# Kernel tuning notes

Hardware: AMD Instinct MI355X
Metric: run time of the kernel (lower is better)

The kernel has to match this reference:

```python
import jax, jax.numpy as jnp
import numpy as np
from jax import lax

PR = [0.0, -39.68, -3.0, 69.12, 39.68, 1.0]  # POINT_CLOUD_RANGE
SIZE = (1024, 1024)  # (W, H)
B = 4
NBF = 64
BN_EPS = 1e-5


def setup_inputs() -> dict:
    key = jax.random.key(0)
    ks = jax.random.split(key, 16)
    N = 800_000
    bidx = jax.random.randint(ks[0], (N,), 0, B).astype(jnp.float32)
    x = jax.random.uniform(ks[1], (N,), minval=PR[0], maxval=PR[3])
    y = jax.random.uniform(ks[2], (N,), minval=PR[1], maxval=PR[4])
    z = jax.random.uniform(ks[3], (N,), minval=PR[2], maxval=PR[5])
    inten = jax.random.uniform(ks[4], (N,))
    points = jnp.stack([bidx, x, y, z, inten], axis=1)
    params = {}
    chans = [(4, 8), (8, 16), (16, 32), (32, NBF)]
    for li, (ci, co) in enumerate(chans, start=1):
        kk = jax.random.split(ks[5 + li], 6)
        params[f"w{li}"] = jax.random.normal(kk[0], (co, ci, 3, 3)) * (1.0 / np.sqrt(ci * 9))
        params[f"b{li}"] = jax.random.normal(kk[1], (co,)) * 0.01
        params[f"g{li}"] = jax.random.uniform(kk[2], (co,), minval=0.5, maxval=1.5)
        params[f"be{li}"] = jax.random.normal(kk[3], (co,)) * 0.01
        params[f"m{li}"] = jax.random.normal(kk[4], (co,)) * 0.01
        params[f"v{li}"] = jax.random.uniform(kk[5], (co,), minval=0.5, maxval=1.5)
    return {"points": points, "batch_size": 4, **params}


def _points_to_bev(points, batch_size):
    # Faithful to points_to_bevs_all (returned channels: count/50, zmin, zmax, intensity;
    # bev_average_z is computed but never returned in the original, so it is omitted).
    W, H = SIZE
    xs = W / (PR[3] - PR[0])
    ys = H / (PR[4] - PR[1])
    # PR[0] == 0 branch of the original
    xp = (points[:, 1] * xs).astype(jnp.int32)
    yp = ((points[:, 2] + (PR[4] - PR[1]) / 2) * ys).astype(jnp.int32)
    b = points[:, 0].astype(jnp.int32)
    mask = (xp >= 0) & (xp < W) & (yp >= 0) & (yp < H)
    lin = jnp.where(mask, (b * H + yp) * W + xp, 0)  # flat [B*H*W] index
    z = points[:, 3]
    inten = points[:, 4]
    n = batch_size * H * W
    neg = jnp.float32(-jnp.inf)
    pos = jnp.float32(jnp.inf)
    cnt = jnp.zeros((n,), jnp.float32).at[lin].add(mask.astype(jnp.float32))
    zmax = jnp.full((n,), -10.0, jnp.float32).at[lin].max(jnp.where(mask, z, neg))
    zmin = jnp.full((n,), 10.0, jnp.float32).at[lin].min(jnp.where(mask, z, pos))
    iv = jnp.zeros((n,), jnp.float32).at[lin].max(jnp.where(mask, inten, neg))
    bev = jnp.where(cnt == 0, 1.0, cnt) / 50.0
    stacked = jnp.stack([bev, zmin, zmax, iv], axis=0).reshape(4, batch_size, H, W)
    return jnp.transpose(stacked, (1, 0, 2, 3))  # [B,4,H,W]


def _cbr(x, w, b, g, be, m, v):
    # Conv(3x3, stride 1, pad 1) + BatchNorm (inference) + ReLU
    y = lax.conv_general_dilated(x, w, (1, 1), 'SAME',
                                 dimension_numbers=('NCHW', 'OIHW', 'NCHW'))
    y = y + b[:, None, None]
    scale = (g / jnp.sqrt(v + BN_EPS))[:, None, None]
    y = (y - m[:, None, None]) * scale + be[:, None, None]
    return jax.nn.relu(y)


def _pool(x):
    return lax.reduce_window(x, -jnp.inf, lax.max, (1, 1, 2, 2), (1, 1, 2, 2), 'VALID')


def reference(points, batch_size,
              w1, b1, g1, be1, m1, v1,
              w2, b2, g2, be2, m2, v2,
              w3, b3, g3, be3, m3, v3,
              w4, b4, g4, be4, m4, v4):
    bev = _points_to_bev(points, batch_size)  # [B,4,1024,1024]
    x = _pool(_cbr(bev, w1, b1, g1, be1, m1, v1))  # [B,8,512,512]
    x = _pool(_cbr(x, w2, b2, g2, be2, m2, v2))    # [B,16,256,256]
    x = _pool(_cbr(x, w3, b3, g3, be3, m3, v3))    # [B,32,128,128]
    return _cbr(x, w4, b4, g4, be4, m4, v4)        # [B,64,128,128] spatial_features
```

## Files before the change

kernel.cpp:

```cpp
#include <hip/hip_runtime.h>
#include <cstdint>
#include <cstddef>

#define HH 1024
#define WW 1024
#define NB 4

typedef _Float16 half8 __attribute__((ext_vector_type(8)));
typedef float f32x4 __attribute__((ext_vector_type(4)));
typedef unsigned long long ull;

__global__ __launch_bounds__(256)
void clear_cells(float4* __restrict__ p, int n4) {
  int stride = gridDim.x * blockDim.x;
  float4 z; z.x = 0.f; z.y = 0.f; z.z = 0.f; z.w = 0.f;
  for (int i = blockIdx.x * blockDim.x + threadIdx.x; i < n4; i += stride)
    p[i] = z;
}

__device__ __forceinline__ unsigned merge_cell(unsigned a, unsigned zq,
                                               unsigned zn, unsigned iq) {
  unsigned cnt = a & 0xFFu;
  unsigned civ = (a >> 8) & 0xFFu;
  unsigned czn = (a >> 16) & 0xFFu;
  unsigned czx = a >> 24;
  cnt = (cnt < 255u) ? cnt + 1u : cnt;
  civ = civ > iq ? civ : iq;
  czn = czn > zn ? czn : zn;
  czx = czx > zq ? czx : zq;
  return cnt | (civ << 8) | (czn << 16) | (czx << 24);
}

__global__ __launch_bounds__(256)
void scatter_points_packed(const float* __restrict__ pts, int n,
                           unsigned* __restrict__ cell) {
  const float xs   = (float)(1024.0 / 69.12);
  const float ys   = (float)(1024.0 / (39.68 + 39.68));
  const float yoff = 39.68f;
  int i = blockIdx.x * blockDim.x + threadIdx.x;
  if (i >= n) return;
  float b  = pts[(size_t)i * 5 + 0];
  float x  = pts[(size_t)i * 5 + 1];
  float y  = pts[(size_t)i * 5 + 2];
  float z  = pts[(size_t)i * 5 + 3];
  float it = pts[(size_t)i * 5 + 4];
  int xp = (int)(x * xs);
  int yp = (int)((y + yoff) * ys);
  if (xp < 0 || xp >= WW || yp < 0 || yp >= HH) return;
  int lin = ((int)b * HH + yp) * WW + xp;

  float zc = fminf(fmaxf(z, -3.f), 1.f);
  unsigned zq = (unsigned)(int)((zc + 3.f) * (255.f / 4.f) + 0.5f);
  if (zq > 255u) zq = 255u;
  float ic = fminf(fmaxf(it, 0.f), 1.f);
  unsigned iq = (unsigned)(int)(ic * 255.f + 0.5f);
  if (iq > 255u) iq = 255u;
  unsigned zn = 255u - zq;

  unsigned g = atomicCAS(&cell[lin], 0u, merge_cell(0u, zq, zn, iq));
  while (g != 0u) {
    unsigned r = atomicCAS(&cell[lin], g, merge_cell(g, zq, zn, iq));
    if (r == g) break;
    g = r;
  }
}

template<int CI, int CIp, int COT, int COp, int HWI, int PXT, int KS,
         bool POOL, int INMODE, bool OUTCL>
__global__ __launch_bounds__(512)
void conv_mfma(const void* __restrict__ in, void* __restrict__ outv,
               const float* __restrict__ wgt, const float* __restrict__ bias,
               const float* __restrict__ gam, const float* __restrict__ bet,
               const float* __restrict__ mean, const float* __restrict__ var) {
  constexpr int PYT  = 32;
  constexpr int NTHR = 512;
  constexpr int NT   = COp / 16;
  constexpr int XH   = PXT / 16;
  constexpr int NCOL = PXT + 2;
  constexpr int NCELL = (PYT + 2) * NCOL;
  constexpr int WROW = KS * 32 + 8;
  constexpr int INE  = NCELL * CIp;
  constexpr int L2C  = (CIp == 8) ? 3 : ((CIp == 16) ? 4 : 5);
  constexpr int KTOT = 9 * CIp;
  constexpr int COR  = (COT < COp) ? COT : COp;
  constexpr int PXH  = PXT / 2;
  constexpr int OCS  = 136;
  static_assert(CIp % 8 == 0 && COp % 16 == 0, "");
  static_assert(!OUTCL || (POOL && COT % 8 == 0), "");
  static_assert(!POOL || 16 * PXH * COp * 2 <= INE * 2, "out overlay fits");
  static_assert(POOL || COp * OCS * 4 <= INE * 2, "out overlay fits");

  __shared__ __align__(16) char s_raw[INE * 2 + COp * WROW * 2 + COp * 8];
  _Float16* s_in = (_Float16*)s_raw;
  _Float16* s_w  = (_Float16*)(s_raw + INE * 2);
  float* s_scale = (float*)(s_raw + INE * 2 + (size_t)COp * WROW * 2);
  float* s_shift = s_scale + COp;

  const int cobase = blockIdx.y * COp;
  const int b = blockIdx.z;
  constexpr int NPX = HWI / PXT;
  const int pyi = blockIdx.x / NPX;
  const int pxi = blockIdx.x - pyi * NPX;
  const int y0 = pyi * PYT, x0 = pxi * PXT;

  half8 zv;
  #pragma unroll
  for (int q = 0; q < 8; ++q) zv[q] = (_Float16)0.f;

  if constexpr (INMODE == 0) {
    const unsigned* pin = (const unsigned*)in;
    for (int t = threadIdx.x; t < NCELL; t += NTHR) {
      int col = t % NCOL;
      int row = t / NCOL;
      int gy = y0 - 1 + row, gx = x0 - 1 + col;
      half8 v = zv;
      if (gy >= 0 && gy < HH && gx >= 0 && gx < WW) {
        unsigned pv = pin[((size_t)b * HH + gy) * WW + gx];
        unsigned cnt = pv & 0xFFu;
        unsigned ivq = (pv >> 8) & 0xFFu;
        unsigned znq = (pv >> 16) & 0xFFu;
        unsigned zxq = pv >> 24;
        float c0, c1, c2, c3;
        if (cnt == 0) { c0 = 0.02f; c1 = 10.f; c2 = -10.f; c3 = 0.f; }
        else {
          c0 = (float)cnt * 0.02f;
          c1 = (float)(255u - znq) * (4.0f / 255.0f) - 3.0f;
          c2 = (float)zxq * (4.0f / 255.0f) - 3.0f;
          c3 = (float)ivq * (1.0f / 255.0f);
        }
        v[0] = (_Float16)c0; v[1] = (_Float16)c1;
        v[2] = (_Float16)c2; v[3] = (_Float16)c3;
      }
      *(half8*)&s_in[(size_t)t * CIp] = v;
    }
  } else {
    const _Float16* fin = (const _Float16*)in;
    for (int t = threadIdx.x; t < NCELL; t += NTHR) {
      int col = t % NCOL;
      int row = t / NCOL;
      int gy = y0 - 1 + row, gx = x0 - 1 + col;
      bool okc = (gy >= 0 && gy < HWI && gx >= 0 && gx < HWI);
      int swz = (CIp == 8) ? 0 : ((CIp == 16) ? ((col >> 2) & 1) : ((col >> 1) & 3));
      #pragma unroll
      for (int c8 = 0; c8 < CIp / 8; ++c8) {
        half8 v = zv;
        if (okc)
          v = *(const half8*)((const _Float16*)fin +
                (((size_t)b * HWI + gy) * HWI + gx) * CI + c8 * 8);
        *(half8*)&s_in[(size_t)t * CIp + ((c8 ^ swz) << 3)] = v;
      }
    }
  }
  for (int t = threadIdx.x; t < COp * KS * 32; t += NTHR) {
    int k   = t % (KS * 32);
    int col = t / (KS * 32);
    int cog = cobase + col;
    float v = 0.f;
    if (k < KTOT && cog < COT) {
      int tap = k / CIp, ci = k % CIp;
      if (ci < CI) v = wgt[((size_t)cog * CI + ci) * 9 + tap];
    }
    s_w[col * WROW + k] = (_Float16)v;
  }
  if (threadIdx.x < COp) {
    int col = threadIdx.x;
    int cog = cobase + col;
    float sc = 0.f, sh = 0.f;
    if (cog < COT) {
      sc = gam[cog] / sqrtf(var[cog] + 1e-5f);
      sh = (bias[cog] - mean[cog]) * sc + bet[cog];
    }
    s_scale[col] = sc; s_shift[col] = sh;
  }
  __syncthreads();

  const int lane = threadIdx.x & 63;
  const int w    = threadIdx.x >> 6;
  const int m    = lane & 15;
  const int hi   = lane >> 4;

  f32x4 acc[4][XH][NT];
  #pragma unroll
  for (int r = 0; r < 4; ++r)
    #pragma unroll
    for (int h = 0; h < XH; ++h)
      #pragma unroll
      for (int n = 0; n < NT; ++n) acc[r][h][n] = 0.f;

  const int y0w = w * 4;
  #pragma unroll
  for (int ks = 0; ks < KS; ++ks) {
    int kc  = ks * 32 + (hi << 3);
    int tap = kc >> L2C;
    if (tap > 8) tap = 8;
    int ci  = kc & (CIp - 1);
    int dy  = (tap * 11) >> 5;
    int dx  = tap - 3 * dy;
    int colA  = m + dx;
    int chunk = ci >> 3;
    int swz = (CIp == 8) ? 0 : ((CIp == 16) ? ((colA >> 2) & 1) : ((colA >> 1) & 3));
    int aoff = ((y0w + dy) * NCOL + colA) * CIp + ((chunk ^ swz) << 3);
    const int boff = m * WROW + ks * 32 + (hi << 3);
    half8 bfr[NT];
    #pragma unroll
    for (int n = 0; n < NT; ++n)
      bfr[n] = *(const half8*)&s_w[boff + n * 16 * WROW];
    #pragma unroll
    for (int r = 0; r < 4; ++r) {
      half8 afr[XH];
      #pragma unroll
      for (int h = 0; h < XH; ++h)
        afr[h] = *(const half8*)&s_in[aoff + r * NCOL * CIp + h * 16 * CIp];
      #pragma unroll
      for (int h = 0; h < XH; ++h)
        #pragma unroll
        for (int n = 0; n < NT; ++n)
          acc[r][h][n] = __builtin_amdgcn_mfma_f32_16x16x32_f16(
              afr[h], bfr[n], acc[r][h][n], 0, 0, 0);
    }
  }

  __syncthreads();

  if constexpr (POOL) {
    _Float16* s_o = (_Float16*)s_raw;
    #pragma unroll
    for (int n = 0; n < NT; ++n) {
      int col = n * 16 + m;
      float sc = s_scale[col], sh = s_shift[col];
      #pragma unroll
      for (int rp = 0; rp < 2; ++rp) {
        #pragma unroll
        for (int h = 0; h < XH; ++h) {
          f32x4 p0 = acc[rp * 2][h][n];
          f32x4 p1 = acc[rp * 2 + 1][h][n];
          float v0 = fmaxf(fmaxf(p0[0], p0[1]), fmaxf(p1[0], p1[1]));
          float v1 = fmaxf(fmaxf(p0[2], p0[3]), fmaxf(p1[2], p1[3]));
          v0 = fmaxf(v0 * sc + sh, 0.f);
          v1 = fmaxf(v1 * sc + sh, 0.f);
          int yp = w * 2 + rp;
          int xp = h * 8 + hi * 2;
          s_o[(yp * PXH + xp) * COp + col]     = (_Float16)v0;
          s_o[(yp * PXH + xp + 1) * COp + col] = (_Float16)v1;
        }
      }
    }
    __syncthreads();
    constexpr int HWO = HWI / 2;
    constexpr int NCHG = (COR + 7) / 8;
    _Float16* og = (_Float16*)outv;
    for (int t = threadIdx.x; t < 16 * PXH * NCHG; t += NTHR) {
      int c8  = t % NCHG;
      int rem = t / NCHG;
      int xp  = rem % PXH;
      int yp  = rem / PXH;
      half8 v = *(const half8*)&s_o[(yp * PXH + xp) * COp + c8 * 8];
      *(half8*)&og[(((size_t)b * HWO + (y0 / 2 + yp)) * HWO + (x0 / 2 + xp)) * COT
                   + cobase + c8 * 8] = v;
    }
  } else {
    float* s_out = (float*)s_raw;
    float* og = (float*)outv;
    #pragma unroll
    for (int r = 0; r < 4; ++r) {
      if (r) __syncthreads();
      #pragma unroll
      for (int n = 0; n < NT; ++n) {
        int col = n * 16 + m;
        float sc = s_scale[col], sh = s_shift[col];
        f32x4 p = acc[r][0][n];
        #pragma unroll
        for (int q = 0; q < 4; ++q) {
          float v = fmaxf(p[q] * sc + sh, 0.f);
          s_out[col * OCS + w * 16 + hi * 4 + q] = v;
        }
      }
      __syncthreads();
      for (int t = threadIdx.x; t < COR * 8 * 16; t += NTHR) {
        int xp = t & 15, ws3 = (t >> 4) & 7, col = t >> 7;
        og[(((size_t)b * COT + cobase + col) * HWI + (y0 + ws3 * 4 + r)) * HWI + (x0 + xp)]
          = s_out[col * OCS + ws3 * 16 + xp];
      }
    }
  }
}

extern "C" void kernel_launch(void* const* d_in, const int* in_sizes, int n_in,
                              void* d_out, int out_size, void* d_ws, size_t ws_size,
                              hipStream_t stream) {
  const float* pts = (const float*)d_in[0];
  const int npts = in_sizes[0] / 5;

  const float* w1  = (const float*)d_in[2];
  const float* b1  = (const float*)d_in[3];
  const float* g1  = (const float*)d_in[4];
  const float* be1 = (const float*)d_in[5];
  const float* m1  = (const float*)d_in[6];
  const float* v1  = (const float*)d_in[7];
  const float* w2  = (const float*)d_in[8];
  const float* b2  = (const float*)d_in[9];
  const float* g2  = (const float*)d_in[10];
  const float* be2 = (const float*)d_in[11];
  const float* m2  = (const float*)d_in[12];
  const float* v2  = (const float*)d_in[13];
  const float* w3  = (const float*)d_in[14];
  const float* b3  = (const float*)d_in[15];
  const float* g3  = (const float*)d_in[16];
  const float* be3 = (const float*)d_in[17];
  const float* m3  = (const float*)d_in[18];
  const float* v3  = (const float*)d_in[19];
  const float* w4  = (const float*)d_in[20];
  const float* b4  = (const float*)d_in[21];
  const float* g4  = (const float*)d_in[22];
  const float* be4 = (const float*)d_in[23];
  const float* m4  = (const float*)d_in[24];
  const float* v4  = (const float*)d_in[25];

  char* ws = (char*)d_ws;
  unsigned* packed = (unsigned*)ws;
  void* l1 = (void*)(ws + 33554432);
  void* l2 = (void*)(ws + 50331648);
  void* l3 = (void*)(ws + 58720256);
  void* outp = d_out;

  clear_cells<<<2048, 256, 0, stream>>>((float4*)packed, (int)((size_t)NB * HH * WW * 4 / 16));
  scatter_points_packed<<<(npts + 255) / 256, 256, 0, stream>>>(pts, npts, packed);

  conv_mfma<4,  8,  8,  16, 1024, 64, 3, true,  0, true ><<<dim3(512, 1, 4), 512, 0, stream>>>(packed, l1, w1, b1, g1, be1, m1, v1);
  conv_mfma<8,  8,  16, 16, 512,  64, 3, true,  1, true ><<<dim3(128, 1, 4), 512, 0, stream>>>(l1,  l2, w2, b2, g2, be2, m2, v2);
  conv_mfma<16, 16, 32, 16, 256,  32, 5, true,  1, true ><<<dim3(64,  2, 4), 512, 0, stream>>>(l2,  l3, w3, b3, g3, be3, m3, v3);
  conv_mfma<32, 32, 64, 16, 128,  16, 9, false, 1, false><<<dim3(32,  4, 4), 512, 0, stream>>>(l3, outp, w4, b4, g4, be4, m4, v4);
}
```

Measured before the change: 101.0 us.

## Pack two horizontal taps per 8-wide K chunk in first conv layer

```diff
diff --git a/kernel.cpp b/kernel.cpp
--- a/kernel.cpp
+++ b/kernel.cpp
@@ -7,6 +7,7 @@
 #define NB 4
 
 typedef _Float16 half8 __attribute__((ext_vector_type(8)));
+typedef _Float16 half4 __attribute__((ext_vector_type(4)));
 typedef float f32x4 __attribute__((ext_vector_type(4)));
 typedef unsigned long long ull;
 
@@ -86,6 +87,7 @@
   constexpr int PXH  = PXT / 2;
   constexpr int OCS  = 136;
   static_assert(CIp % 8 == 0 && COp % 16 == 0, "");
+  static_assert(INMODE != 0 || (CI == 4 && CIp == 8 && KS == 2), "");
   static_assert(!OUTCL || (POOL && COT % 8 == 0), "");
   static_assert(!POOL || 16 * PXH * COp * 2 <= INE * 2, "out overlay fits");
   static_assert(POOL || COp * OCS * 4 <= INE * 2, "out overlay fits");
@@ -113,7 +115,9 @@
       int col = t % NCOL;
       int row = t / NCOL;
       int gy = y0 - 1 + row, gx = x0 - 1 + col;
-      half8 v = zv;
+      half4 v;
+      v[0] = (_Float16)0.f; v[1] = (_Float16)0.f;
+      v[2] = (_Float16)0.f; v[3] = (_Float16)0.f;
       if (gy >= 0 && gy < HH && gx >= 0 && gx < WW) {
         unsigned pv = pin[((size_t)b * HH + gy) * WW + gx];
         unsigned cnt = pv & 0xFFu;
@@ -131,7 +135,15 @@
         v[0] = (_Float16)c0; v[1] = (_Float16)c1;
         v[2] = (_Float16)c2; v[3] = (_Float16)c3;
       }
-      *(half8*)&s_in[(size_t)t * CIp] = v;
+      *(half4*)&s_in[(size_t)t * 8] = v;
+      if (col > 0)
+        *(half4*)&s_in[(size_t)(t - 1) * 8 + 4] = v;
+      if (col == NCOL - 1) {
+        half4 z4;
+        z4[0] = (_Float16)0.f; z4[1] = (_Float16)0.f;
+        z4[2] = (_Float16)0.f; z4[3] = (_Float16)0.f;
+        *(half4*)&s_in[(size_t)t * 8 + 4] = z4;
+      }
     }
   } else {
     const _Float16* fin = (const _Float16*)in;
@@ -151,16 +163,33 @@
       }
     }
   }
-  for (int t = threadIdx.x; t < COp * KS * 32; t += NTHR) {
-    int k   = t % (KS * 32);
-    int col = t / (KS * 32);
-    int cog = cobase + col;
-    float v = 0.f;
-    if (k < KTOT && cog < COT) {
-      int tap = k / CIp, ci = k % CIp;
-      if (ci < CI) v = wgt[((size_t)cog * CI + ci) * 9 + tap];
-    }
-    s_w[col * WROW + k] = (_Float16)v;
+  if constexpr (INMODE == 0) {
+    for (int t = threadIdx.x; t < COp * KS * 32; t += NTHR) {
+      int k   = t % (KS * 32);
+      int col = t / (KS * 32);
+      int cog = cobase + col;
+      int p = k >> 3, j = k & 7;
+      float v = 0.f;
+      if (p < 6 && cog < COT) {
+        int tA = p + ((p + 1) >> 1);
+        int ci = j & 3;
+        if (j < 4) v = wgt[((size_t)cog * CI + ci) * 9 + tA];
+        else if ((p & 1) == 0) v = wgt[((size_t)cog * CI + ci) * 9 + tA + 1];
+      }
+      s_w[col * WROW + k] = (_Float16)v;
+    }
+  } else {
+    for (int t = threadIdx.x; t < COp * KS * 32; t += NTHR) {
+      int k   = t % (KS * 32);
+      int col = t / (KS * 32);
+      int cog = cobase + col;
+      float v = 0.f;
+      if (k < KTOT && cog < COT) {
+        int tap = k / CIp, ci = k % CIp;
+        if (ci < CI) v = wgt[((size_t)cog * CI + ci) * 9 + tap];
+      }
+      s_w[col * WROW + k] = (_Float16)v;
+    }
   }
   if (threadIdx.x < COp) {
     int col = threadIdx.x;
@@ -190,16 +219,25 @@
   const int y0w = w * 4;
   #pragma unroll
   for (int ks = 0; ks < KS; ++ks) {
-    int kc  = ks * 32 + (hi << 3);
-    int tap = kc >> L2C;
-    if (tap > 8) tap = 8;
-    int ci  = kc & (CIp - 1);
-    int dy  = (tap * 11) >> 5;
-    int dx  = tap - 3 * dy;
-    int colA  = m + dx;
-    int chunk = ci >> 3;
-    int swz = (CIp == 8) ? 0 : ((CIp == 16) ? ((colA >> 2) & 1) : ((colA >> 1) & 3));
-    int aoff = ((y0w + dy) * NCOL + colA) * CIp + ((chunk ^ swz) << 3);
+    int aoff;
+    if constexpr (INMODE == 0) {
+      int p = ks * 4 + hi;
+      if (p > 5) p = 5;
+      int dy  = p >> 1;
+      int dxA = (p & 1) << 1;
+      aoff = ((y0w + dy) * NCOL + m + dxA) * 8;
+    } else {
+      int kc  = ks * 32 + (hi << 3);
+      int tap = kc >> L2C;
+      if (tap > 8) tap = 8;
+      int ci  = kc & (CIp - 1);
+      int dy  = (tap * 11) >> 5;
+      int dx  = tap - 3 * dy;
+      int colA  = m + dx;
+      int chunk = ci >> 3;
+      int swz = (CIp == 8) ? 0 : ((CIp == 16) ? ((colA >> 2) & 1) : ((colA >> 1) & 3));
+      aoff = ((y0w + dy) * NCOL + colA) * CIp + ((chunk ^ swz) << 3);
+    }
     const int boff = m * WROW + ks * 32 + (hi << 3);
     half8 bfr[NT];
     #pragma unroll
@@ -326,7 +364,7 @@
   clear_cells<<<2048, 256, 0, stream>>>((float4*)packed, (int)((size_t)NB * HH * WW * 4 / 16));
   scatter_points_packed<<<(npts + 255) / 256, 256, 0, stream>>>(pts, npts, packed);
 
-  conv_mfma<4,  8,  8,  16, 1024, 64, 3, true,  0, true ><<<dim3(512, 1, 4), 512, 0, stream>>>(packed, l1, w1, b1, g1, be1, m1, v1);
+  conv_mfma<4,  8,  8,  16, 1024, 64, 2, true,  0, true ><<<dim3(512, 1, 4), 512, 0, stream>>>(packed, l1, w1, b1, g1, be1, m1, v1);
   conv_mfma<8,  8,  16, 16, 512,  64, 3, true,  1, true ><<<dim3(128, 1, 4), 512, 0, stream>>>(l1,  l2, w2, b2, g2, be2, m2, v2);
   conv_mfma<16, 16, 32, 16, 256,  32, 5, true,  1, true ><<<dim3(64,  2, 4), 512, 0, stream>>>(l2,  l3, w3, b3, g3, be3, m3, v3);
   conv_mfma<32, 32, 64, 16, 128,  16, 9, false, 1, false><<<dim3(32,  4, 4), 512, 0, stream>>>(l3, outp, w4, b4, g4, be4, m4, v4);
```

After: 95.38 us. 1.06x faster.
